# Kernel tuning notes

Measured on AMD Instinct MI355X. Metric: run time of the kernel, lower is better.

## Reference

```python
import jax, jax.numpy as jnp
import numpy as np

THRESHOLD = 1.0
BETA_INIT = 0.9

def setup_inputs() -> dict:
    key = jax.random.key(0)
    k1, k2 = jax.random.split(key)
    B, T, D, E = 16, 4096, 1024, 64
    seq = jax.random.normal(k1, (B, T, D), dtype=jnp.float32)
    W = jax.random.normal(k2, (E, D), dtype=jnp.float32) * (1.0 / np.sqrt(D))
    b = jnp.zeros((E,), dtype=jnp.float32)
    logit = float(np.log(BETA_INIT / (1.0 - BETA_INIT)))
    beta_raw = jnp.full((E,), logit, dtype=jnp.float32)
    return {"seq": seq, "W": W, "b": b, "beta_raw": beta_raw}

def reference(seq, W, b, beta_raw):
    # seq: [B,T,D], W: [E,D], b: [E], beta_raw: [E]
    B, T, D = seq.shape
    E = W.shape[0]
    beta = jax.nn.sigmoid(beta_raw)                       # [E]
    # batch the per-timestep Linear into one GEMM: [B,T,E]
    I = jnp.einsum('btd,ed->bte', seq, W) + b
    def step(U, I_t):
        U = beta * U + I_t                                # leaky integrate
        U = U - jax.nn.relu(U - THRESHOLD)                # soft reset (clip at threshold)
        return U, None
    U0 = jnp.zeros((B, E), dtype=seq.dtype)
    # scan over time: I transposed to [T,B,E]
    U_final, _ = jax.lax.scan(step, U0, jnp.swapaxes(I, 0, 1))
    return jax.nn.softmax(U_final, axis=-1)
```

## Files before the change

kernel.cpp:

```cpp
#include <hip/hip_runtime.h>
#include <hip/hip_bf16.h>
#include <cstdint>

#define B_ 16
#define T_ 4096
#define D_ 1024
#define E_ 64
#define THRESH 1.0f

#define MBLK 128
#define BK 64
#define PAD_K 72

typedef float f32x4 __attribute__((ext_vector_type(4)));
typedef short s16x8 __attribute__((ext_vector_type(8)));

__device__ __forceinline__ void split1(float v, unsigned short& h, unsigned short& l) {
    unsigned u = __float_as_uint(v);
    float hf = __uint_as_float(u & 0xFFFF0000u);
    float r = v - hf;
    h = (unsigned short)(u >> 16);
    l = (unsigned short)(__float_as_uint(r) >> 16);
}

__global__ void wconv_kernel(const float* __restrict__ W,
                             unsigned short* __restrict__ Whi,
                             unsigned short* __restrict__ Wlo) {
    int i = (blockIdx.x * 256 + threadIdx.x) * 4;
    if (i >= E_ * D_) return;
    float4 v = *reinterpret_cast<const float4*>(W + i);
    ushort4 h, l;
    split1(v.x, h.x, l.x); split1(v.y, h.y, l.y);
    split1(v.z, h.z, l.z); split1(v.w, h.w, l.w);
    *reinterpret_cast<ushort4*>(Whi + i) = h;
    *reinterpret_cast<ushort4*>(Wlo + i) = l;
}

__global__ __launch_bounds__(256, 2) void lif_gemm_kernel(
    const float* __restrict__ seq,
    const unsigned short* __restrict__ Whi, const unsigned short* __restrict__ Wlo,
    const float* __restrict__ bias, const float* __restrict__ beta_raw,
    float* __restrict__ Cw, float* __restrict__ Mw)
{
    __shared__ __align__(16) unsigned char lds[36864 + 18432];
    unsigned short* Ahi  = (unsigned short*)lds;
    unsigned short* Alo  = (unsigned short*)(lds + 18432);
    unsigned short* WhiL = (unsigned short*)(lds + 36864);
    unsigned short* WloL = (unsigned short*)(lds + 36864 + 9216);

    const int tid  = threadIdx.x;
    const int wave = tid >> 6;
    const int lane = tid & 63;
    const long row0 = (long)blockIdx.x * MBLK;

    f32x4 acc[2][4] = {};

    for (int k0 = 0; k0 < D_; k0 += BK) {
        __syncthreads();
        #pragma unroll
        for (int i = 0; i < 8; ++i) {
            int linear = i * 256 + tid;
            int r  = linear >> 4;
            int kk = (linear & 15) << 2;
            float4 v = *reinterpret_cast<const float4*>(seq + (row0 + r) * D_ + k0 + kk);
            ushort4 h, l;
            split1(v.x, h.x, l.x); split1(v.y, h.y, l.y);
            split1(v.z, h.z, l.z); split1(v.w, h.w, l.w);
            *reinterpret_cast<ushort4*>(Ahi + r * PAD_K + kk) = h;
            *reinterpret_cast<ushort4*>(Alo + r * PAD_K + kk) = l;
        }
        #pragma unroll
        for (int i = 0; i < 2; ++i) {
            int linear = i * 256 + tid;
            int r  = linear >> 3;
            int kk = (linear & 7) << 3;
            uint4 vh = *reinterpret_cast<const uint4*>(Whi + r * D_ + k0 + kk);
            uint4 vl = *reinterpret_cast<const uint4*>(Wlo + r * D_ + k0 + kk);
            *reinterpret_cast<uint4*>(WhiL + r * PAD_K + kk) = vh;
            *reinterpret_cast<uint4*>(WloL + r * PAD_K + kk) = vl;
        }
        __syncthreads();
        #pragma unroll
        for (int ks = 0; ks < BK; ks += 32) {
            const int kf = ks + ((lane >> 4) << 3);
            s16x8 ah[2], al[2], bh[4], bl[4];
            #pragma unroll
            for (int m = 0; m < 2; ++m) {
                int tr = wave * 32 + m * 16 + (lane & 15);
                ah[m] = *reinterpret_cast<const s16x8*>(Ahi + tr * PAD_K + kf);
                al[m] = *reinterpret_cast<const s16x8*>(Alo + tr * PAD_K + kf);
            }
            #pragma unroll
            for (int n = 0; n < 4; ++n) {
                int er = n * 16 + (lane & 15);
                bh[n] = *reinterpret_cast<const s16x8*>(WhiL + er * PAD_K + kf);
                bl[n] = *reinterpret_cast<const s16x8*>(WloL + er * PAD_K + kf);
            }
            #pragma unroll
            for (int m = 0; m < 2; ++m)
                #pragma unroll
                for (int n = 0; n < 4; ++n)
                    acc[m][n] = __builtin_amdgcn_mfma_f32_16x16x32_bf16(ah[m], bh[n], acc[m][n], 0, 0, 0);
            #pragma unroll
            for (int m = 0; m < 2; ++m)
                #pragma unroll
                for (int n = 0; n < 4; ++n)
                    acc[m][n] = __builtin_amdgcn_mfma_f32_16x16x32_bf16(al[m], bh[n], acc[m][n], 0, 0, 0);
            #pragma unroll
            for (int m = 0; m < 2; ++m)
                #pragma unroll
                for (int n = 0; n < 4; ++n)
                    acc[m][n] = __builtin_amdgcn_mfma_f32_16x16x32_bf16(ah[m], bl[n], acc[m][n], 0, 0, 0);
        }
    }
    __syncthreads();

    float* Iw = (float*)(lds + wave * 8192);
    #pragma unroll
    for (int m = 0; m < 2; ++m)
        #pragma unroll
        for (int n = 0; n < 4; ++n) {
            int e  = n * 16 + (lane & 15);
            int tl = m * 16 + ((lane >> 4) << 2);
            #pragma unroll
            for (int r = 0; r < 4; ++r)
                Iw[(tl + r) * 64 + e] = acc[m][n][r];
        }

    const float be   = bias[lane];
    const float beta = 1.0f / (1.0f + __expf(-beta_raw[lane]));
    float Cc = 0.0f;
    float Mm = 3.0e38f;
    #pragma unroll
    for (int t = 0; t < 32; ++t) {
        float v = Iw[t * 64 + lane] + be;
        Cc = fmaf(beta, Cc, v);
        Mm = fminf(fmaf(beta, Mm, v), THRESH);
    }
    int sub = blockIdx.x * 4 + wave;
    Cw[sub * 64 + lane] = Cc;
    Mw[sub * 64 + lane] = Mm;
}

__global__ void lif_combine_kernel(const float* __restrict__ Cw, const float* __restrict__ Mw,
                                   const float* __restrict__ beta_raw, float* __restrict__ out)
{
    int b = blockIdx.x;
    int e = threadIdx.x;
    float beta = 1.0f / (1.0f + __expf(-beta_raw[e]));
    float A = beta * beta;
    A = A * A;
    A = A * A;
    A = A * A;
    A = A * A;
    float U = 0.0f;
    const float* Cp = Cw + (size_t)b * 128 * 64 + e;
    const float* Mp = Mw + (size_t)b * 128 * 64 + e;
    #pragma unroll 8
    for (int c = 0; c < 128; ++c)
        U = fminf(fmaf(A, U, Cp[c * 64]), Mp[c * 64]);
    float m = U;
    #pragma unroll
    for (int off = 32; off; off >>= 1) m = fmaxf(m, __shfl_xor(m, off, 64));
    float ex = __expf(U - m);
    float s = ex;
    #pragma unroll
    for (int off = 32; off; off >>= 1) s += __shfl_xor(s, off, 64);
    out[b * 64 + e] = ex / s;
}

extern "C" void kernel_launch(void* const* d_in, const int* in_sizes, int n_in,
                              void* d_out, int out_size, void* d_ws, size_t ws_size,
                              hipStream_t stream)
{
    const float* seq  = (const float*)d_in[0];
    const float* W    = (const float*)d_in[1];
    const float* bias = (const float*)d_in[2];
    const float* braw = (const float*)d_in[3];
    float* out = (float*)d_out;

    char* ws = (char*)d_ws;
    unsigned short* Whi = (unsigned short*)ws;
    unsigned short* Wlo = (unsigned short*)(ws + 131072);
    float* Cw = (float*)(ws + 262144);
    float* Mw = (float*)(ws + 786432);

    wconv_kernel<<<64, 256, 0, stream>>>(W, Whi, Wlo);
    lif_gemm_kernel<<<(B_ * T_) / MBLK, 256, 0, stream>>>(seq, Whi, Wlo, bias, braw, Cw, Mw);
    lif_combine_kernel<<<B_, E_, 0, stream>>>(Cw, Mw, braw, out);
}
```

Baseline: 61.84 us.

## Load GEMM operands directly from global into registers, drop LDS and W preconversion

The GEMM kernel no longer stages seq and W tiles through LDS with barriers. Each lane loads its MFMA fragment straight from global memory and splits it into bf16 hi/lo in registers, and W is split on the fly, which removes the separate wconv kernel launch. The per-wave time scan is now done directly on accumulator registers using shuffle-based segment combining instead of an LDS transpose. The tradeoff is that each block re-reads and re-splits all of W from global/L2, and the per-lane loads are strided across rows and less coalesced.

Measured after the change: 101.4 us. 1.64x slower.

```diff
diff --git a/kernel.cpp b/kernel.cpp
--- a/kernel.cpp
+++ b/kernel.cpp
@@ -7,10 +7,7 @@
 #define D_ 1024
 #define E_ 64
 #define THRESH 1.0f
-
 #define MBLK 128
-#define BK 64
-#define PAD_K 72
 
 typedef float f32x4 __attribute__((ext_vector_type(4)));
 typedef short s16x8 __attribute__((ext_vector_type(8)));
@@ -23,123 +20,125 @@
     l = (unsigned short)(__float_as_uint(r) >> 16);
 }
 
-__global__ void wconv_kernel(const float* __restrict__ W,
-                             unsigned short* __restrict__ Whi,
-                             unsigned short* __restrict__ Wlo) {
-    int i = (blockIdx.x * 256 + threadIdx.x) * 4;
-    if (i >= E_ * D_) return;
-    float4 v = *reinterpret_cast<const float4*>(W + i);
-    ushort4 h, l;
-    split1(v.x, h.x, l.x); split1(v.y, h.y, l.y);
-    split1(v.z, h.z, l.z); split1(v.w, h.w, l.w);
-    *reinterpret_cast<ushort4*>(Whi + i) = h;
-    *reinterpret_cast<ushort4*>(Wlo + i) = l;
+__device__ __forceinline__ void split8(float4 v0, float4 v1, s16x8& h8, s16x8& l8) {
+    unsigned short h0,h1,h2,h3,h4,h5,h6,h7, l0,l1,l2,l3,l4,l5,l6,l7;
+    split1(v0.x,h0,l0); split1(v0.y,h1,l1); split1(v0.z,h2,l2); split1(v0.w,h3,l3);
+    split1(v1.x,h4,l4); split1(v1.y,h5,l5); split1(v1.z,h6,l6); split1(v1.w,h7,l7);
+    h8 = (s16x8){(short)h0,(short)h1,(short)h2,(short)h3,(short)h4,(short)h5,(short)h6,(short)h7};
+    l8 = (s16x8){(short)l0,(short)l1,(short)l2,(short)l3,(short)l4,(short)l5,(short)l6,(short)l7};
 }
 
 __global__ __launch_bounds__(256, 2) void lif_gemm_kernel(
-    const float* __restrict__ seq,
-    const unsigned short* __restrict__ Whi, const unsigned short* __restrict__ Wlo,
+    const float* __restrict__ seq, const float* __restrict__ W,
     const float* __restrict__ bias, const float* __restrict__ beta_raw,
     float* __restrict__ Cw, float* __restrict__ Mw)
 {
-    __shared__ __align__(16) unsigned char lds[36864 + 18432];
-    unsigned short* Ahi  = (unsigned short*)lds;
-    unsigned short* Alo  = (unsigned short*)(lds + 18432);
-    unsigned short* WhiL = (unsigned short*)(lds + 36864);
-    unsigned short* WloL = (unsigned short*)(lds + 36864 + 9216);
-
     const int tid  = threadIdx.x;
     const int wave = tid >> 6;
     const int lane = tid & 63;
-    const long row0 = (long)blockIdx.x * MBLK;
+    const int c = lane & 15;
+    const int q = lane >> 4;
+
+    const float* a0 = seq + ((long)blockIdx.x * MBLK + wave * 32 + c) * D_ + q * 8;
+    const float* w0 = W + c * D_ + q * 8;
 
     f32x4 acc[2][4] = {};
 
-    for (int k0 = 0; k0 < D_; k0 += BK) {
-        __syncthreads();
+    #pragma unroll 4
+    for (int ks = 0; ks < 32; ++ks) {
+        const int kb = ks * 32;
+        s16x8 ah[2], al[2], bh[4], bl[4];
         #pragma unroll
-        for (int i = 0; i < 8; ++i) {
-            int linear = i * 256 + tid;
-            int r  = linear >> 4;
-            int kk = (linear & 15) << 2;
-            float4 v = *reinterpret_cast<const float4*>(seq + (row0 + r) * D_ + k0 + kk);
-            ushort4 h, l;
-            split1(v.x, h.x, l.x); split1(v.y, h.y, l.y);
-            split1(v.z, h.z, l.z); split1(v.w, h.w, l.w);
-            *reinterpret_cast<ushort4*>(Ahi + r * PAD_K + kk) = h;
-            *reinterpret_cast<ushort4*>(Alo + r * PAD_K + kk) = l;
+        for (int m = 0; m < 2; ++m) {
+            float4 v0 = *reinterpret_cast<const float4*>(a0 + m * 16 * D_ + kb);
+            float4 v1 = *reinterpret_cast<const float4*>(a0 + m * 16 * D_ + kb + 4);
+            split8(v0, v1, ah[m], al[m]);
         }
         #pragma unroll
-        for (int i = 0; i < 2; ++i) {
-            int linear = i * 256 + tid;
-            int r  = linear >> 3;
-            int kk = (linear & 7) << 3;
-            uint4 vh = *reinterpret_cast<const uint4*>(Whi + r * D_ + k0 + kk);
-            uint4 vl = *reinterpret_cast<const uint4*>(Wlo + r * D_ + k0 + kk);
-            *reinterpret_cast<uint4*>(WhiL + r * PAD_K + kk) = vh;
-            *reinterpret_cast<uint4*>(WloL + r * PAD_K + kk) = vl;
+        for (int n = 0; n < 4; ++n) {
+            float4 v0 = *reinterpret_cast<const float4*>(w0 + n * 16 * D_ + kb);
+            float4 v1 = *reinterpret_cast<const float4*>(w0 + n * 16 * D_ + kb + 4);
+            split8(v0, v1, bh[n], bl[n]);
         }
-        __syncthreads();
         #pragma unroll
-        for (int ks = 0; ks < BK; ks += 32) {
-            const int kf = ks + ((lane >> 4) << 3);
-            s16x8 ah[2], al[2], bh[4], bl[4];
+        for (int m = 0; m < 2; ++m)
             #pragma unroll
-            for (int m = 0; m < 2; ++m) {
-                int tr = wave * 32 + m * 16 + (lane & 15);
-                ah[m] = *reinterpret_cast<const s16x8*>(Ahi + tr * PAD_K + kf);
-                al[m] = *reinterpret_cast<const s16x8*>(Alo + tr * PAD_K + kf);
-            }
+            for (int n = 0; n < 4; ++n)
+                acc[m][n] = __builtin_amdgcn_mfma_f32_16x16x32_bf16(ah[m], bh[n], acc[m][n], 0, 0, 0);
+        #pragma unroll
+        for (int m = 0; m < 2; ++m)
             #pragma unroll
-            for (int n = 0; n < 4; ++n) {
-                int er = n * 16 + (lane & 15);
-                bh[n] = *reinterpret_cast<const s16x8*>(WhiL + er * PAD_K + kf);
-                bl[n] = *reinterpret_cast<const s16x8*>(WloL + er * PAD_K + kf);
-            }
+            for (int n = 0; n < 4; ++n)
+                acc[m][n] = __builtin_amdgcn_mfma_f32_16x16x32_bf16(al[m], bh[n], acc[m][n], 0, 0, 0);
+        #pragma unroll
+        for (int m = 0; m < 2; ++m)
             #pragma unroll
-            for (int m = 0; m < 2; ++m)
-                #pragma unroll
-                for (int n = 0; n < 4; ++n)
-                    acc[m][n] = __builtin_amdgcn_mfma_f32_16x16x32_bf16(ah[m], bh[n], acc[m][n], 0, 0, 0);
-            #pragma unroll
-            for (int m = 0; m < 2; ++m)
-                #pragma unroll
-                for (int n = 0; n < 4; ++n)
-                    acc[m][n] = __builtin_amdgcn_mfma_f32_16x16x32_bf16(al[m], bh[n], acc[m][n], 0, 0, 0);
-            #pragma unroll
-            for (int m = 0; m < 2; ++m)
-                #pragma unroll
-                for (int n = 0; n < 4; ++n)
-                    acc[m][n] = __builtin_amdgcn_mfma_f32_16x16x32_bf16(ah[m], bl[n], acc[m][n], 0, 0, 0);
-        }
+            for (int n = 0; n < 4; ++n)
+                acc[m][n] = __builtin_amdgcn_mfma_f32_16x16x32_bf16(ah[m], bl[n], acc[m][n], 0, 0, 0);
     }
-    __syncthreads();
 
-    float* Iw = (float*)(lds + wave * 8192);
+    float beta[4], A4[4], A8[4], bi[4];
+    #pragma unroll
+    for (int n = 0; n < 4; ++n) {
+        beta[n] = 1.0f / (1.0f + __expf(-beta_raw[n * 16 + c]));
+        float b2 = beta[n] * beta[n];
+        A4[n] = b2 * b2;
+        A8[n] = A4[n] * A4[n];
+        bi[n] = bias[n * 16 + c];
+    }
+
+    float C[2][4], M[2][4];
     #pragma unroll
     for (int m = 0; m < 2; ++m)
         #pragma unroll
         for (int n = 0; n < 4; ++n) {
-            int e  = n * 16 + (lane & 15);
-            int tl = m * 16 + ((lane >> 4) << 2);
+            float Cc = 0.0f, Mm = 3.0e38f;
             #pragma unroll
-            for (int r = 0; r < 4; ++r)
-                Iw[(tl + r) * 64 + e] = acc[m][n][r];
+            for (int r = 0; r < 4; ++r) {
+                float v = acc[m][n][r] + bi[n];
+                Cc = fmaf(beta[n], Cc, v);
+                Mm = fminf(fmaf(beta[n], Mm, v), THRESH);
+            }
+            C[m][n] = Cc; M[m][n] = Mm;
         }
 
-    const float be   = bias[lane];
-    const float beta = 1.0f / (1.0f + __expf(-beta_raw[lane]));
-    float Cc = 0.0f;
-    float Mm = 3.0e38f;
     #pragma unroll
-    for (int t = 0; t < 32; ++t) {
-        float v = Iw[t * 64 + lane] + be;
-        Cc = fmaf(beta, Cc, v);
-        Mm = fminf(fmaf(beta, Mm, v), THRESH);
+    for (int m = 0; m < 2; ++m)
+        #pragma unroll
+        for (int n = 0; n < 4; ++n) {
+            {
+                float Cp = __shfl_xor(C[m][n], 16, 64);
+                float Mp = __shfl_xor(M[m][n], 16, 64);
+                bool sf = (lane & 16) == 0;
+                float Cf = sf ? C[m][n] : Cp, Cs = sf ? Cp : C[m][n];
+                float Mf = sf ? M[m][n] : Mp, Ms = sf ? Mp : M[m][n];
+                C[m][n] = fmaf(A4[n], Cf, Cs);
+                M[m][n] = fminf(fmaf(A4[n], Mf, Cs), Ms);
+            }
+            {
+                float Cp = __shfl_xor(C[m][n], 32, 64);
+                float Mp = __shfl_xor(M[m][n], 32, 64);
+                bool sf = (lane & 32) == 0;
+                float Cf = sf ? C[m][n] : Cp, Cs = sf ? Cp : C[m][n];
+                float Mf = sf ? M[m][n] : Mp, Ms = sf ? Mp : M[m][n];
+                C[m][n] = fmaf(A8[n], Cf, Cs);
+                M[m][n] = fminf(fmaf(A8[n], Mf, Cs), Ms);
+            }
+        }
+
+    float Cm[4], Mm4[4];
+    #pragma unroll
+    for (int n = 0; n < 4; ++n) {
+        float A16 = A8[n] * A8[n];
+        Cm[n]  = fmaf(A16, C[0][n], C[1][n]);
+        Mm4[n] = fminf(fmaf(A16, M[0][n], C[1][n]), M[1][n]);
     }
+
+    float Co = (q == 0) ? Cm[0] : (q == 1) ? Cm[1] : (q == 2) ? Cm[2] : Cm[3];
+    float Mo = (q == 0) ? Mm4[0] : (q == 1) ? Mm4[1] : (q == 2) ? Mm4[2] : Mm4[3];
     int sub = blockIdx.x * 4 + wave;
-    Cw[sub * 64 + lane] = Cc;
-    Mw[sub * 64 + lane] = Mm;
+    Cw[sub * 64 + q * 16 + c] = Co;
+    Mw[sub * 64 + q * 16 + c] = Mo;
 }
 
 __global__ void lif_combine_kernel(const float* __restrict__ Cw, const float* __restrict__ Mw,
@@ -157,8 +156,8 @@
     const float* Cp = Cw + (size_t)b * 128 * 64 + e;
     const float* Mp = Mw + (size_t)b * 128 * 64 + e;
     #pragma unroll 8
-    for (int c = 0; c < 128; ++c)
-        U = fminf(fmaf(A, U, Cp[c * 64]), Mp[c * 64]);
+    for (int cch = 0; cch < 128; ++cch)
+        U = fminf(fmaf(A, U, Cp[cch * 64]), Mp[cch * 64]);
     float m = U;
     #pragma unroll
     for (int off = 32; off; off >>= 1) m = fmaxf(m, __shfl_xor(m, off, 64));
@@ -180,12 +179,9 @@
     float* out = (float*)d_out;
 
     char* ws = (char*)d_ws;
-    unsigned short* Whi = (unsigned short*)ws;
-    unsigned short* Wlo = (unsigned short*)(ws + 131072);
-    float* Cw = (float*)(ws + 262144);
-    float* Mw = (float*)(ws + 786432);
+    float* Cw = (float*)ws;
+    float* Mw = (float*)(ws + 524288);
 
-    wconv_kernel<<<64, 256, 0, stream>>>(W, Whi, Wlo);
-    lif_gemm_kernel<<<(B_ * T_) / MBLK, 256, 0, stream>>>(seq, Whi, Wlo, bias, braw, Cw, Mw);
+    lif_gemm_kernel<<<(B_ * T_) / MBLK, 256, 0, stream>>>(seq, W, bias, braw, Cw, Mw);
     lif_combine_kernel<<<B_, E_, 0, stream>>>(Cw, Mw, braw, out);
 }
```
